# Kernel optimization log

Hardware: AMD Instinct MI355X
Metric: run time of the kernel (lower is better)

The kernel has to match this reference:

```python
import jax, jax.numpy as jnp
import numpy as np

CHUNK = 128  # single steady-state chunk tier (T divisible by 128)
DECAY_MIN = 0.005


def setup_inputs() -> dict:
    key = jax.random.key(0)
    k0, k1, k2, k3, k4 = jax.random.split(key, 5)
    B, H, T, K = 4, 16, 2048, 64
    r = jax.random.normal(k0, (B, H, T, K), jnp.float32) * 0.5
    k = jax.random.normal(k1, (B, H, T, K), jnp.float32) * 0.5
    v = jax.random.normal(k2, (B, H, T, K), jnp.float32)
    # log-space decay (negative); mild magnitude keeps exp() of cumulative
    # in-chunk decays within fp32 range (torch original upcasts to fp64)
    w = -(jax.random.uniform(k3, (B, H, T, K), jnp.float32) * 0.2 + 0.01)
    u = jax.random.normal(k4, (1, H, 1, K), jnp.float32) * 0.5
    wkv_state = jnp.zeros((B, H, K, K), jnp.float32)
    return {"r": r, "k": k, "v": v, "w": w, "u": u, "wkv_state": wkv_state}


def _chunked_wkv(r, k, v, w, u, wkv_state):
    B, H, T, K = r.shape
    Tc = CHUNK
    N = T // Tc
    # decay preprocessing (log space)
    w_decay = jnp.clip(jnp.exp(w), DECAY_MIN, None)
    w_log = jnp.log(w_decay)
    wc = w_log.reshape(B, H, N, Tc, K)
    wc_cum = jnp.cumsum(wc, axis=-2)                       # inclusive cumsum
    shifted = jnp.pad(wc_cum[..., :-1, :], ((0, 0), (0, 0), (0, 0), (1, 0), (0, 0)))
    ws = wc.sum(axis=-2, keepdims=True)                    # (B,H,N,1,K)
    w_inter = jnp.exp(ws - wc_cum)                          # (B,H,N,Tc,K)
    w_intra = jnp.exp(wc_cum - wc)
    ws_e = jnp.exp(jnp.swapaxes(ws, -1, -2))               # (B,H,N,K,1)

    rc = r.reshape(B, H, N, Tc, K)
    kc = k.reshape(B, H, N, Tc, K)
    vc = v.reshape(B, H, N, Tc, K)

    # numerically-centered intra-chunk decays (offset at chunk midpoint)
    off = shifted[..., Tc // 2:Tc // 2 + 1, :]
    r_dec = jnp.exp(shifted - off)
    k_inv = jnp.exp(off - wc_cum)

    # intra-chunk attention: strictly-lower-triangular + u-bonus diagonal
    a = jnp.einsum('bhnik,bhnjk->bhnij', rc * r_dec, kc * k_inv)
    a = jnp.tril(a, -1)
    diag = jnp.einsum('bhntk,bhntk->bhnt', rc, u[:, :, None] * kc)
    a = a + diag[..., :, None] * jnp.eye(Tc, dtype=a.dtype)
    out = jnp.einsum('bhnij,bhnjv->bhniv', a, vc)

    # inter-chunk: sequential state carry via scan
    wkv = jnp.einsum('bhntk,bhntv->bhnkv', kc * w_inter, vc)   # (B,H,N,K,K)

    def step(state, inp):
        ws_i, wkv_i = inp
        return state * ws_i + wkv_i, state

    ws_s = jnp.moveaxis(ws_e, 2, 0)    # (N,B,H,K,1)
    wkv_s = jnp.moveaxis(wkv, 2, 0)    # (N,B,H,K,K)
    final_state, states = jax.lax.scan(step, wkv_state, (ws_s, wkv_s))
    states = jnp.moveaxis(states, 0, 2)  # (B,H,N,K,K) — state entering chunk n

    out = out + jnp.einsum('bhntk,bhnkv->bhntv', rc * w_intra, states)
    return out.reshape(B, H, T, K), final_state


def reference(r, k, v, w, u, wkv_state):
    return _chunked_wkv(r, k, v, w, u, wkv_state)
```

## Files before the change

kernel.cpp:

```cpp
#include <hip/hip_runtime.h>

#define TC 128
#define KD 64
#define WLOG_MIN (-5.2983174f)

typedef __attribute__((ext_vector_type(8))) short short8;
typedef __attribute__((ext_vector_type(4))) short short4_t;
typedef __attribute__((ext_vector_type(4))) float f32x4;

__device__ __forceinline__ unsigned short f2bf(float x) {
  union { float f; unsigned int u; } c; c.f = x;
  unsigned int u = c.u + 0x7fffu + ((c.u >> 16) & 1u);
  return (unsigned short)(u >> 16);
}
__device__ __forceinline__ float bf2f(unsigned short x) {
  union { unsigned int u; float f; } c; c.u = ((unsigned int)x) << 16; return c.f;
}
__device__ __forceinline__ f32x4 shfl4(f32x4 v, int src) {
  f32x4 r;
  #pragma unroll
  for (int i = 0; i < 4; ++i) r[i] = __shfl(v[i], src, 64);
  return r;
}


__global__ __launch_bounds__(512, 8)
void rwkv_wkv(const float* __restrict__ kk_, const float* __restrict__ vv,
              const float* __restrict__ ww,
              unsigned short* __restrict__ wkv_u16, float* __restrict__ wse_ws,
              int N) {
  __shared__ alignas(16) unsigned short vT_s[KD * TC];
  __shared__ alignas(16) unsigned short kiT_s[KD * TC];
  __shared__ alignas(16) float segtot[8 * 64];

  const int bid = blockIdx.x;
  const int n = bid % N, bh = bid / N;
  const size_t base = ((size_t)bh * N + n) * (TC * KD);
  const float *kg = kk_ + base, *vg = vv + base, *wg = ww + base;

  const int tid = threadIdx.x;
  const int lane = tid & 63, wv = tid >> 6;
  const int q = lane >> 4, c4 = lane & 15, kd0 = c4 * 4;

  f32x4 wl4[4];
  #pragma unroll
  for (int j = 0; j < 4; ++j) {
    const int t = wv * 16 + q * 4 + j;
    wl4[j] = *(const f32x4*)&wg[t * KD + kd0];
  }
  #pragma unroll
  for (int j = 0; j < 4; ++j)
    #pragma unroll
    for (int i = 0; i < 4; ++i) wl4[j][i] = fmaxf(wl4[j][i], WLOG_MIN);

  const f32x4 ls = ((wl4[0] + wl4[1]) + wl4[2]) + wl4[3];
  const f32x4 s0 = shfl4(ls, c4), s1 = shfl4(ls, 16 + c4);
  const f32x4 s2 = shfl4(ls, 32 + c4), s3 = shfl4(ls, 48 + c4);
  const f32x4 zero = {0.f, 0.f, 0.f, 0.f};
  f32x4 pre = (q > 0 ? s0 : zero);
  pre += (q > 1 ? s1 : zero);
  pre += (q > 2 ? s2 : zero);
  const f32x4 tot = ((s0 + s1) + s2) + s3;
  if (q == 0) *(f32x4*)&segtot[wv * 64 + kd0] = tot;
  __syncthreads();

  f32x4 segofs4 = zero, myoff4 = zero, wsum4 = zero;
  #pragma unroll
  for (int i = 0; i < 8; ++i) {
    const f32x4 si = *(const f32x4*)&segtot[i * 64 + kd0];
    if (i < wv) segofs4 += si;
    if (i < 4) myoff4 += si;
    wsum4 += si;
  }
  f32x4 wsoff4;
  #pragma unroll
  for (int i = 0; i < 4; ++i) wsoff4[i] = __expf(wsum4[i] - myoff4[i]);
  if (wv == 0 && q == 0) {
    f32x4 e;
    #pragma unroll
    for (int i = 0; i < 4; ++i) e[i] = __expf(wsum4[i]);
    *(f32x4*)&wse_ws[((size_t)bh * N + n) * KD + kd0] = e;
  }

  {
    f32x4 cc = segofs4 + pre;
    short4_t kib[4], vb[4];
    #pragma unroll
    for (int j = 0; j < 4; ++j) {
      const int t = wv * 16 + q * 4 + j;
      const f32x4 k4j = *(const f32x4*)&kg[t * KD + kd0];
      const f32x4 v4j = *(const f32x4*)&vg[t * KD + kd0];
      #pragma unroll
      for (int i = 0; i < 4; ++i) {
        kib[i][j] = (short)f2bf(k4j[i] * __expf(myoff4[i] - cc[i] - wl4[j][i]));
        vb[i][j] = (short)f2bf(v4j[i]);
      }
      cc += wl4[j];
    }
    const int g = wv * 2 + (q >> 1), p4 = (q & 1) * 4;
    #pragma unroll
    for (int i = 0; i < 4; ++i) {
      const int kd = kd0 + i;
      *(short4_t*)&kiT_s[kd * TC + ((g ^ (kd & 7)) << 3) + p4] = kib[i];
      *(short4_t*)&vT_s[kd * TC + ((g ^ (kd & 7)) << 3) + p4] = vb[i];
    }
  }
  __syncthreads();

  {
    const int quad = lane >> 4, l16 = lane & 15;
    const int kt = wv >> 1;
    const int nb = (wv & 1) * 2;
    f32x4 acc[2] = {{0,0,0,0},{0,0,0,0}};
    const int row = kt * 16 + l16;
    #pragma unroll
    for (int ks = 0; ks < 4; ++ks) {
      short8 a = *(const short8*)&kiT_s[row * TC + (((ks * 4 + quad) ^ (row & 7)) << 3)];
      #pragma unroll
      for (int nn = 0; nn < 2; ++nn) {
        const int vd = (nb + nn) * 16 + l16;
        short8 b = *(const short8*)&vT_s[vd * TC + (((ks * 4 + quad) ^ (vd & 7)) << 3)];
        acc[nn] = __builtin_amdgcn_mfma_f32_16x16x32_bf16(a, b, acc[nn], 0, 0, 0);
      }
    }
    float wso[4];
    #pragma unroll
    for (int reg = 0; reg < 4; ++reg) wso[reg] = __shfl(wsoff4[reg], kt * 4 + quad, 64);
    unsigned short* wkvg = wkv_u16 + ((size_t)bh * N + n) * (KD * KD);
    #pragma unroll
    for (int nn = 0; nn < 2; ++nn)
      #pragma unroll
      for (int reg = 0; reg < 4; ++reg)
        wkvg[(kt * 16 + quad * 4 + reg) * KD + (nb + nn) * 16 + l16] = f2bf(acc[nn][reg] * wso[reg]);
  }
}

__global__ __launch_bounds__(512, 4)
void rwkv_main(const float* __restrict__ rr, const float* __restrict__ kk_,
               const float* __restrict__ vv, const float* __restrict__ ww,
               const float* __restrict__ uu,
               const unsigned short* __restrict__ wkv_u16,
               const float* __restrict__ wse_ws,
               const float* __restrict__ st_in,
               float* __restrict__ out, float* __restrict__ final_out,
               int H, int N) {
  __shared__ alignas(16) unsigned short rd_s[TC * KD];
  __shared__ alignas(16) unsigned short ki_s[TC * KD];
  __shared__ alignas(16) unsigned short vT_s[KD * TC];
  __shared__ alignas(16) unsigned short diag_s[TC];
  float* segtot = (float*)rd_s;

  const int bid = blockIdx.x;
  const int n = bid % N, bh = bid / N, h = bh % H;
  const size_t base = ((size_t)bh * N + n) * (TC * KD);
  const float *rg = rr + base, *kg = kk_ + base, *vg = vv + base, *wg = ww + base;

  const int tid = threadIdx.x;
  const int lane = tid & 63, wv = tid >> 6;
  const int q = lane >> 4, c4 = lane & 15, kd0 = c4 * 4;
  const int quad = lane >> 4, l16 = lane & 15;
  const f32x4 uk4 = *(const f32x4*)&uu[h * KD + kd0];

  f32x4 wl4[4], r4[4], k4[4], v4[4];
  #pragma unroll
  for (int j = 0; j < 4; ++j) {
    const int t = wv * 16 + q * 4 + j;
    wl4[j] = *(const f32x4*)&wg[t * KD + kd0];
    r4[j] = *(const f32x4*)&rg[t * KD + kd0];
    k4[j] = *(const f32x4*)&kg[t * KD + kd0];
    v4[j] = *(const f32x4*)&vg[t * KD + kd0];
  }
  #pragma unroll
  for (int j = 0; j < 4; ++j)
    #pragma unroll
    for (int i = 0; i < 4; ++i) wl4[j][i] = fmaxf(wl4[j][i], WLOG_MIN);

  const f32x4 ls = ((wl4[0] + wl4[1]) + wl4[2]) + wl4[3];
  const f32x4 s0 = shfl4(ls, c4), s1 = shfl4(ls, 16 + c4);
  const f32x4 s2 = shfl4(ls, 32 + c4), s3 = shfl4(ls, 48 + c4);
  const f32x4 zero = {0.f, 0.f, 0.f, 0.f};
  f32x4 pre = (q > 0 ? s0 : zero);
  pre += (q > 1 ? s1 : zero);
  pre += (q > 2 ? s2 : zero);
  const f32x4 tot = ((s0 + s1) + s2) + s3;
  if (q == 0) *(f32x4*)&segtot[wv * 64 + kd0] = tot;
  __syncthreads();
  f32x4 segofs4 = zero, myoff4 = zero;
  #pragma unroll
  for (int i = 0; i < 8; ++i) {
    const f32x4 si = *(const f32x4*)&segtot[i * 64 + kd0];
    if (i < wv) segofs4 += si;
    if (i < 4) myoff4 += si;
  }
  __syncthreads();
  f32x4 eoff4;
  #pragma unroll
  for (int i = 0; i < 4; ++i) eoff4[i] = __expf(myoff4[i]);

  short4_t rwq[4];
  {
    f32x4 cc = segofs4 + pre;
    short4_t vb[4];
    float dar[4];
    #pragma unroll
    for (int j = 0; j < 4; ++j) {
      const int t = wv * 16 + q * 4 + j;
      const int addr = t * KD + (((c4 >> 1) ^ (t & 7) ^ ((t >> 3) & 7)) << 3) + (c4 & 1) * 4;
      short4_t rdv, kiv;
      #pragma unroll
      for (int i = 0; i < 4; ++i) {
        const float e1 = __expf(cc[i] - myoff4[i]);
        rdv[i] = (short)f2bf(r4[j][i] * e1);
        rwq[j][i] = (short)f2bf(r4[j][i] * e1 * eoff4[i]);
        kiv[i] = (short)f2bf(k4[j][i] * __expf(myoff4[i] - cc[i] - wl4[j][i]));
        vb[i][j] = (short)f2bf(v4[j][i]);
      }
      *(short4_t*)&rd_s[addr] = rdv;
      *(short4_t*)&ki_s[addr] = kiv;
      dar[j] = r4[j][0] * uk4[0] * k4[j][0];
      dar[j] += r4[j][1] * uk4[1] * k4[j][1];
      dar[j] += r4[j][2] * uk4[2] * k4[j][2];
      dar[j] += r4[j][3] * uk4[3] * k4[j][3];
      cc += wl4[j];
    }
    const int g = wv * 2 + (q >> 1), p4 = (q & 1) * 4;
    #pragma unroll
    for (int i = 0; i < 4; ++i) {
      const int kd = kd0 + i;
      *(short4_t*)&vT_s[kd * TC + ((g ^ (kd & 7)) << 3) + p4] = vb[i];
    }
    #pragma unroll
    for (int o = 8; o > 0; o >>= 1)
      #pragma unroll
      for (int j = 0; j < 4; ++j) dar[j] += __shfl_xor(dar[j], o, 64);
    if (c4 == 0) {
      short4_t dp;
      #pragma unroll
      for (int j = 0; j < 4; ++j) dp[j] = (short)f2bf(dar[j]);
      *(short4_t*)&diag_s[wv * 16 + q * 4] = dp;
    }
  }
  __syncthreads();

  const int skd = tid >> 3, sv0 = (tid & 7) * 8;
  const size_t sbase = (size_t)bh * (KD * KD);
  float s[8];
  *(f32x4*)&s[0] = *(const f32x4*)&st_in[sbase + skd * KD + sv0];
  *(f32x4*)&s[4] = *(const f32x4*)&st_in[sbase + skd * KD + sv0 + 4];
  const float* wseb = wse_ws + (size_t)bh * N * KD + skd;
  const unsigned short* wkvb = wkv_u16 + (size_t)bh * N * (KD * KD) + skd * KD + sv0;
  {
    float e_c = 0.f; short8 x_c = {0};
    if (n > 0) {
      e_c = wseb[0];
      x_c = *(const short8*)&wkvb[0];
    }
    for (int j = 0; j < n; ++j) {
      const float e = e_c; const short8 x = x_c;
      if (j + 1 < n) {
        e_c = wseb[(size_t)(j + 1) * KD];
        x_c = *(const short8*)&wkvb[(size_t)(j + 1) * (KD * KD)];
      }
      #pragma unroll
      for (int i = 0; i < 8; ++i) s[i] = s[i] * e + bf2f((unsigned short)x[i]);
    }
  }

  f32x4 oacc[4];
  {
    const int ib = wv, i0 = ib * 16, irow = i0 + l16;
    const int rsw = (irow & 7) ^ ((irow >> 3) & 7);
    short8 b0 = *(const short8*)&rd_s[irow * KD + ((quad ^ rsw) << 3)];
    short8 b1 = *(const short8*)&rd_s[irow * KD + (((4 + quad) ^ rsw) << 3)];
    const float diag_i = bf2f(diag_s[irow]);
    #pragma unroll
    for (int nn = 0; nn < 4; ++nn) oacc[nn] = (f32x4){0, 0, 0, 0};
    const int npairs = (ib + 2) >> 1;
    unsigned short* astw = &rd_s[wv * 16 * KD];
    for (int jp = 0; jp < npairs; ++jp) {
      #pragma unroll
      for (int jj = 0; jj < 2; ++jj) {
        const int j = jp * 2 + jj;
        short4_t pk;
        if (j <= ib) {
          const int jrow = j * 16 + l16;
          const int jsw = (jrow & 7) ^ ((jrow >> 3) & 7);
          short8 a0 = *(const short8*)&ki_s[jrow * KD + ((quad ^ jsw) << 3)];
          short8 a1 = *(const short8*)&ki_s[jrow * KD + (((4 + quad) ^ jsw) << 3)];
          f32x4 at = {0, 0, 0, 0};
          at = __builtin_amdgcn_mfma_f32_16x16x32_bf16(a0, b0, at, 0, 0, 0);
          at = __builtin_amdgcn_mfma_f32_16x16x32_bf16(a1, b1, at, 0, 0, 0);
          #pragma unroll
          for (int reg = 0; reg < 4; ++reg) {
            const int je = j * 16 + quad * 4 + reg;
            float val = at[reg];
            if (j == ib) val = (je < irow) ? val : ((je == irow) ? diag_i : 0.f);
            pk[reg] = (short)f2bf(val);
          }
        } else {
          pk = (short4_t)0;
        }
        *(short4_t*)&astw[l16 * 40 + jj * 16 + quad * 4] = pk;
      }
      short8 af = *(const short8*)&astw[l16 * 40 + quad * 8];
      #pragma unroll
      for (int nn = 0; nn < 4; ++nn) {
        const int vd = nn * 16 + l16;
        short8 bv = *(const short8*)&vT_s[vd * TC + (((jp * 4 + quad) ^ (vd & 7)) << 3)];
        oacc[nn] = __builtin_amdgcn_mfma_f32_16x16x32_bf16(af, bv, oacc[nn], 0, 0, 0);
      }
    }
  }
  __syncthreads();

  {
    const int g = skd >> 3, k7 = skd & 7;
    #pragma unroll
    for (int i = 0; i < 8; ++i) {
      const int vd = sv0 + i;
      ki_s[vd * KD + (((g ^ (vd & 7)) << 3) | k7)] = f2bf(s[i]);
    }
  }
  #pragma unroll
  for (int j = 0; j < 4; ++j) {
    const int t = wv * 16 + q * 4 + j;
    const int addr = t * KD + (((c4 >> 1) ^ (t & 7) ^ ((t >> 3) & 7)) << 3) + (c4 & 1) * 4;
    *(short4_t*)&rd_s[addr] = rwq[j];
  }
  if (n == N - 1) {
    const float e = wseb[(size_t)n * KD];
    const short8 x = *(const short8*)&wkvb[(size_t)n * (KD * KD)];
    #pragma unroll
    for (int i = 0; i < 8; ++i) s[i] = s[i] * e + bf2f((unsigned short)x[i]);
    *(f32x4*)&final_out[sbase + skd * KD + sv0] = *(const f32x4*)&s[0];
    *(f32x4*)&final_out[sbase + skd * KD + sv0 + 4] = *(const f32x4*)&s[4];
  }
  __syncthreads();

  {
    const int ib = wv, trow = ib * 16 + l16;
    const int rsw = (trow & 7) ^ ((trow >> 3) & 7);
    short8 a0 = *(const short8*)&rd_s[trow * KD + ((quad ^ rsw) << 3)];
    short8 a1 = *(const short8*)&rd_s[trow * KD + (((4 + quad) ^ rsw) << 3)];
    float* og = out + base;
    #pragma unroll
    for (int nn = 0; nn < 4; ++nn) {
      const int vd = nn * 16 + l16;
      short8 b0 = *(const short8*)&ki_s[vd * KD + ((quad ^ (vd & 7)) << 3)];
      short8 b1 = *(const short8*)&ki_s[vd * KD + (((4 + quad) ^ (vd & 7)) << 3)];
      f32x4 acc = {0, 0, 0, 0};
      acc = __builtin_amdgcn_mfma_f32_16x16x32_bf16(a0, b0, acc, 0, 0, 0);
      acc = __builtin_amdgcn_mfma_f32_16x16x32_bf16(a1, b1, acc, 0, 0, 0);
      #pragma unroll
      for (int reg = 0; reg < 4; ++reg)
        og[(size_t)(ib * 16 + quad * 4 + reg) * KD + nn * 16 + l16] = oacc[nn][reg] + acc[reg];
    }
  }
}

extern "C" void kernel_launch(void* const* d_in, const int* in_sizes, int n_in,
                              void* d_out, int out_size, void* d_ws, size_t ws_size,
                              hipStream_t stream) {
  const float* r = (const float*)d_in[0];
  const float* k = (const float*)d_in[1];
  const float* v = (const float*)d_in[2];
  const float* w = (const float*)d_in[3];
  const float* u = (const float*)d_in[4];
  const float* st0 = (const float*)d_in[5];
  float* out = (float*)d_out;

  const int BH = in_sizes[5] / (KD * KD);
  const int H = in_sizes[4] / KD;
  const int T = in_sizes[0] / (BH * KD);
  const int N = T / TC;

  unsigned short* wkv_u16 = (unsigned short*)d_ws;
  float* wse_ws = (float*)(wkv_u16 + (size_t)BH * N * KD * KD);
  float* final_out = out + (size_t)in_sizes[0];

  rwkv_wkv<<<BH * N, 512, 0, stream>>>(k, v, w, wkv_u16, wse_ws, N);
  rwkv_main<<<BH * N, 512, 0, stream>>>(r, k, v, w, u, wkv_u16, wse_ws, st0,
                                        out, final_out, H, N);
}
```

Baseline: 204.2 us.

## Process two consecutive chunks per block to halve state prefix recomputation

Each main-kernel block now handles a pair of adjacent chunks, rebuilding the carried state once for the first chunk and advancing it by one step for the second. This cuts the grid in half and roughly halves the redundant sequential state-prefix loads and FMAs summed over all blocks. In exchange the chunks inside a block run serially with extra barriers, and there are half as many blocks to hide latency (1024 to 512 blocks). The code assumes N is even.

```diff
diff --git a/kernel.cpp b/kernel.cpp
--- a/kernel.cpp
+++ b/kernel.cpp
@@ -150,97 +150,16 @@
   __shared__ alignas(16) unsigned short diag_s[TC];
   float* segtot = (float*)rd_s;
 
+  const int np = N >> 1;
   const int bid = blockIdx.x;
-  const int n = bid % N, bh = bid / N, h = bh % H;
-  const size_t base = ((size_t)bh * N + n) * (TC * KD);
-  const float *rg = rr + base, *kg = kk_ + base, *vg = vv + base, *wg = ww + base;
+  const int p = bid % np, bh = bid / np, h = bh % H;
+  const int n0 = 2 * p, n1 = n0 + 1;
 
   const int tid = threadIdx.x;
   const int lane = tid & 63, wv = tid >> 6;
   const int q = lane >> 4, c4 = lane & 15, kd0 = c4 * 4;
   const int quad = lane >> 4, l16 = lane & 15;
   const f32x4 uk4 = *(const f32x4*)&uu[h * KD + kd0];
-
-  f32x4 wl4[4], r4[4], k4[4], v4[4];
-  #pragma unroll
-  for (int j = 0; j < 4; ++j) {
-    const int t = wv * 16 + q * 4 + j;
-    wl4[j] = *(const f32x4*)&wg[t * KD + kd0];
-    r4[j] = *(const f32x4*)&rg[t * KD + kd0];
-    k4[j] = *(const f32x4*)&kg[t * KD + kd0];
-    v4[j] = *(const f32x4*)&vg[t * KD + kd0];
-  }
-  #pragma unroll
-  for (int j = 0; j < 4; ++j)
-    #pragma unroll
-    for (int i = 0; i < 4; ++i) wl4[j][i] = fmaxf(wl4[j][i], WLOG_MIN);
-
-  const f32x4 ls = ((wl4[0] + wl4[1]) + wl4[2]) + wl4[3];
-  const f32x4 s0 = shfl4(ls, c4), s1 = shfl4(ls, 16 + c4);
-  const f32x4 s2 = shfl4(ls, 32 + c4), s3 = shfl4(ls, 48 + c4);
-  const f32x4 zero = {0.f, 0.f, 0.f, 0.f};
-  f32x4 pre = (q > 0 ? s0 : zero);
-  pre += (q > 1 ? s1 : zero);
-  pre += (q > 2 ? s2 : zero);
-  const f32x4 tot = ((s0 + s1) + s2) + s3;
-  if (q == 0) *(f32x4*)&segtot[wv * 64 + kd0] = tot;
-  __syncthreads();
-  f32x4 segofs4 = zero, myoff4 = zero;
-  #pragma unroll
-  for (int i = 0; i < 8; ++i) {
-    const f32x4 si = *(const f32x4*)&segtot[i * 64 + kd0];
-    if (i < wv) segofs4 += si;
-    if (i < 4) myoff4 += si;
-  }
-  __syncthreads();
-  f32x4 eoff4;
-  #pragma unroll
-  for (int i = 0; i < 4; ++i) eoff4[i] = __expf(myoff4[i]);
-
-  short4_t rwq[4];
-  {
-    f32x4 cc = segofs4 + pre;
-    short4_t vb[4];
-    float dar[4];
-    #pragma unroll
-    for (int j = 0; j < 4; ++j) {
-      const int t = wv * 16 + q * 4 + j;
-      const int addr = t * KD + (((c4 >> 1) ^ (t & 7) ^ ((t >> 3) & 7)) << 3) + (c4 & 1) * 4;
-      short4_t rdv, kiv;
-      #pragma unroll
-      for (int i = 0; i < 4; ++i) {
-        const float e1 = __expf(cc[i] - myoff4[i]);
-        rdv[i] = (short)f2bf(r4[j][i] * e1);
-        rwq[j][i] = (short)f2bf(r4[j][i] * e1 * eoff4[i]);
-        kiv[i] = (short)f2bf(k4[j][i] * __expf(myoff4[i] - cc[i] - wl4[j][i]));
-        vb[i][j] = (short)f2bf(v4[j][i]);
-      }
-      *(short4_t*)&rd_s[addr] = rdv;
-      *(short4_t*)&ki_s[addr] = kiv;
-      dar[j] = r4[j][0] * uk4[0] * k4[j][0];
-      dar[j] += r4[j][1] * uk4[1] * k4[j][1];
-      dar[j] += r4[j][2] * uk4[2] * k4[j][2];
-      dar[j] += r4[j][3] * uk4[3] * k4[j][3];
-      cc += wl4[j];
-    }
-    const int g = wv * 2 + (q >> 1), p4 = (q & 1) * 4;
-    #pragma unroll
-    for (int i = 0; i < 4; ++i) {
-      const int kd = kd0 + i;
-      *(short4_t*)&vT_s[kd * TC + ((g ^ (kd & 7)) << 3) + p4] = vb[i];
-    }
-    #pragma unroll
-    for (int o = 8; o > 0; o >>= 1)
-      #pragma unroll
-      for (int j = 0; j < 4; ++j) dar[j] += __shfl_xor(dar[j], o, 64);
-    if (c4 == 0) {
-      short4_t dp;
-      #pragma unroll
-      for (int j = 0; j < 4; ++j) dp[j] = (short)f2bf(dar[j]);
-      *(short4_t*)&diag_s[wv * 16 + q * 4] = dp;
-    }
-  }
-  __syncthreads();
 
   const int skd = tid >> 3, sv0 = (tid & 7) * 8;
   const size_t sbase = (size_t)bh * (KD * KD);
@@ -251,13 +170,13 @@
   const unsigned short* wkvb = wkv_u16 + (size_t)bh * N * (KD * KD) + skd * KD + sv0;
   {
     float e_c = 0.f; short8 x_c = {0};
-    if (n > 0) {
+    if (n0 > 0) {
       e_c = wseb[0];
       x_c = *(const short8*)&wkvb[0];
     }
-    for (int j = 0; j < n; ++j) {
+    for (int j = 0; j < n0; ++j) {
       const float e = e_c; const short8 x = x_c;
-      if (j + 1 < n) {
+      if (j + 1 < n0) {
         e_c = wseb[(size_t)(j + 1) * KD];
         x_c = *(const short8*)&wkvb[(size_t)(j + 1) * (KD * KD)];
       }
@@ -265,96 +184,193 @@
       for (int i = 0; i < 8; ++i) s[i] = s[i] * e + bf2f((unsigned short)x[i]);
     }
   }
-
-  f32x4 oacc[4];
-  {
-    const int ib = wv, i0 = ib * 16, irow = i0 + l16;
-    const int rsw = (irow & 7) ^ ((irow >> 3) & 7);
-    short8 b0 = *(const short8*)&rd_s[irow * KD + ((quad ^ rsw) << 3)];
-    short8 b1 = *(const short8*)&rd_s[irow * KD + (((4 + quad) ^ rsw) << 3)];
-    const float diag_i = bf2f(diag_s[irow]);
-    #pragma unroll
-    for (int nn = 0; nn < 4; ++nn) oacc[nn] = (f32x4){0, 0, 0, 0};
-    const int npairs = (ib + 2) >> 1;
-    unsigned short* astw = &rd_s[wv * 16 * KD];
-    for (int jp = 0; jp < npairs; ++jp) {
-      #pragma unroll
-      for (int jj = 0; jj < 2; ++jj) {
-        const int j = jp * 2 + jj;
-        short4_t pk;
-        if (j <= ib) {
-          const int jrow = j * 16 + l16;
-          const int jsw = (jrow & 7) ^ ((jrow >> 3) & 7);
-          short8 a0 = *(const short8*)&ki_s[jrow * KD + ((quad ^ jsw) << 3)];
-          short8 a1 = *(const short8*)&ki_s[jrow * KD + (((4 + quad) ^ jsw) << 3)];
-          f32x4 at = {0, 0, 0, 0};
-          at = __builtin_amdgcn_mfma_f32_16x16x32_bf16(a0, b0, at, 0, 0, 0);
-          at = __builtin_amdgcn_mfma_f32_16x16x32_bf16(a1, b1, at, 0, 0, 0);
-          #pragma unroll
-          for (int reg = 0; reg < 4; ++reg) {
-            const int je = j * 16 + quad * 4 + reg;
-            float val = at[reg];
-            if (j == ib) val = (je < irow) ? val : ((je == irow) ? diag_i : 0.f);
-            pk[reg] = (short)f2bf(val);
+  const float en0 = wseb[(size_t)n0 * KD];
+  const short8 xn0 = *(const short8*)&wkvb[(size_t)n0 * (KD * KD)];
+
+  auto do_chunk = [&](int n, const float* s8) {
+    const size_t base = ((size_t)bh * N + n) * (TC * KD);
+    const float *rg = rr + base, *kg = kk_ + base, *vg = vv + base, *wg = ww + base;
+
+    f32x4 wl4[4], r4[4], k4[4], v4[4];
+    #pragma unroll
+    for (int j = 0; j < 4; ++j) {
+      const int t = wv * 16 + q * 4 + j;
+      wl4[j] = *(const f32x4*)&wg[t * KD + kd0];
+      r4[j] = *(const f32x4*)&rg[t * KD + kd0];
+      k4[j] = *(const f32x4*)&kg[t * KD + kd0];
+      v4[j] = *(const f32x4*)&vg[t * KD + kd0];
+    }
+    #pragma unroll
+    for (int j = 0; j < 4; ++j)
+      #pragma unroll
+      for (int i = 0; i < 4; ++i) wl4[j][i] = fmaxf(wl4[j][i], WLOG_MIN);
+
+    const f32x4 ls = ((wl4[0] + wl4[1]) + wl4[2]) + wl4[3];
+    const f32x4 s0 = shfl4(ls, c4), s1 = shfl4(ls, 16 + c4);
+    const f32x4 s2 = shfl4(ls, 32 + c4), s3 = shfl4(ls, 48 + c4);
+    const f32x4 zero = {0.f, 0.f, 0.f, 0.f};
+    f32x4 pre = (q > 0 ? s0 : zero);
+    pre += (q > 1 ? s1 : zero);
+    pre += (q > 2 ? s2 : zero);
+    const f32x4 tot = ((s0 + s1) + s2) + s3;
+    if (q == 0) *(f32x4*)&segtot[wv * 64 + kd0] = tot;
+    __syncthreads();
+    f32x4 segofs4 = zero, myoff4 = zero;
+    #pragma unroll
+    for (int i = 0; i < 8; ++i) {
+      const f32x4 si = *(const f32x4*)&segtot[i * 64 + kd0];
+      if (i < wv) segofs4 += si;
+      if (i < 4) myoff4 += si;
+    }
+    __syncthreads();
+    f32x4 eoff4;
+    #pragma unroll
+    for (int i = 0; i < 4; ++i) eoff4[i] = __expf(myoff4[i]);
+
+    short4_t rwq[4];
+    {
+      f32x4 cc = segofs4 + pre;
+      short4_t vb[4];
+      float dar[4];
+      #pragma unroll
+      for (int j = 0; j < 4; ++j) {
+        const int t = wv * 16 + q * 4 + j;
+        const int addr = t * KD + (((c4 >> 1) ^ (t & 7) ^ ((t >> 3) & 7)) << 3) + (c4 & 1) * 4;
+        short4_t rdv, kiv;
+        #pragma unroll
+        for (int i = 0; i < 4; ++i) {
+          const float e1 = __expf(cc[i] - myoff4[i]);
+          rdv[i] = (short)f2bf(r4[j][i] * e1);
+          rwq[j][i] = (short)f2bf(r4[j][i] * e1 * eoff4[i]);
+          kiv[i] = (short)f2bf(k4[j][i] * __expf(myoff4[i] - cc[i] - wl4[j][i]));
+          vb[i][j] = (short)f2bf(v4[j][i]);
+        }
+        *(short4_t*)&rd_s[addr] = rdv;
+        *(short4_t*)&ki_s[addr] = kiv;
+        dar[j] = r4[j][0] * uk4[0] * k4[j][0];
+        dar[j] += r4[j][1] * uk4[1] * k4[j][1];
+        dar[j] += r4[j][2] * uk4[2] * k4[j][2];
+        dar[j] += r4[j][3] * uk4[3] * k4[j][3];
+        cc += wl4[j];
+      }
+      const int g = wv * 2 + (q >> 1), p4 = (q & 1) * 4;
+      #pragma unroll
+      for (int i = 0; i < 4; ++i) {
+        const int kd = kd0 + i;
+        *(short4_t*)&vT_s[kd * TC + ((g ^ (kd & 7)) << 3) + p4] = vb[i];
+      }
+      #pragma unroll
+      for (int o = 8; o > 0; o >>= 1)
+        #pragma unroll
+        for (int j = 0; j < 4; ++j) dar[j] += __shfl_xor(dar[j], o, 64);
+      if (c4 == 0) {
+        short4_t dp;
+        #pragma unroll
+        for (int j = 0; j < 4; ++j) dp[j] = (short)f2bf(dar[j]);
+        *(short4_t*)&diag_s[wv * 16 + q * 4] = dp;
+      }
+    }
+    __syncthreads();
+
+    f32x4 oacc[4];
+    {
+      const int ib = wv, i0 = ib * 16, irow = i0 + l16;
+      const int rsw = (irow & 7) ^ ((irow >> 3) & 7);
+      short8 b0 = *(const short8*)&rd_s[irow * KD + ((quad ^ rsw) << 3)];
+      short8 b1 = *(const short8*)&rd_s[irow * KD + (((4 + quad) ^ rsw) << 3)];
+      const float diag_i = bf2f(diag_s[irow]);
+      #pragma unroll
+      for (int nn = 0; nn < 4; ++nn) oacc[nn] = (f32x4){0, 0, 0, 0};
+      const int npairs = (ib + 2) >> 1;
+      unsigned short* astw = &rd_s[wv * 16 * KD];
+      for (int jp = 0; jp < npairs; ++jp) {
+        #pragma unroll
+        for (int jj = 0; jj < 2; ++jj) {
+          const int j = jp * 2 + jj;
+          short4_t pk;
+          if (j <= ib) {
+            const int jrow = j * 16 + l16;
+            const int jsw = (jrow & 7) ^ ((jrow >> 3) & 7);
+            short8 a0 = *(const short8*)&ki_s[jrow * KD + ((quad ^ jsw) << 3)];
+            short8 a1 = *(const short8*)&ki_s[jrow * KD + (((4 + quad) ^ jsw) << 3)];
+            f32x4 at = {0, 0, 0, 0};
+            at = __builtin_amdgcn_mfma_f32_16x16x32_bf16(a0, b0, at, 0, 0, 0);
+            at = __builtin_amdgcn_mfma_f32_16x16x32_bf16(a1, b1, at, 0, 0, 0);
+            #pragma unroll
+            for (int reg = 0; reg < 4; ++reg) {
+              const int je = j * 16 + quad * 4 + reg;
+              float val = at[reg];
+              if (j == ib) val = (je < irow) ? val : ((je == irow) ? diag_i : 0.f);
+              pk[reg] = (short)f2bf(val);
+            }
+          } else {
+            pk = (short4_t)0;
           }
-        } else {
-          pk = (short4_t)0;
+          *(short4_t*)&astw[l16 * 40 + jj * 16 + quad * 4] = pk;
         }
-        *(short4_t*)&astw[l16 * 40 + jj * 16 + quad * 4] = pk;
-      }
-      short8 af = *(const short8*)&astw[l16 * 40 + quad * 8];
+        short8 af = *(const short8*)&astw[l16 * 40 + quad * 8];
+        #pragma unroll
+        for (int nn = 0; nn < 4; ++nn) {
+          const int vd = nn * 16 + l16;
+          short8 bv = *(const short8*)&vT_s[vd * TC + (((jp * 4 + quad) ^ (vd & 7)) << 3)];
+          oacc[nn] = __builtin_amdgcn_mfma_f32_16x16x32_bf16(af, bv, oacc[nn], 0, 0, 0);
+        }
+      }
+    }
+    __syncthreads();
+
+    {
+      const int g = skd >> 3, k7 = skd & 7;
+      #pragma unroll
+      for (int i = 0; i < 8; ++i) {
+        const int vd = sv0 + i;
+        ki_s[vd * KD + (((g ^ (vd & 7)) << 3) | k7)] = f2bf(s8[i]);
+      }
+    }
+    #pragma unroll
+    for (int j = 0; j < 4; ++j) {
+      const int t = wv * 16 + q * 4 + j;
+      const int addr = t * KD + (((c4 >> 1) ^ (t & 7) ^ ((t >> 3) & 7)) << 3) + (c4 & 1) * 4;
+      *(short4_t*)&rd_s[addr] = rwq[j];
+    }
+    __syncthreads();
+
+    {
+      const int ib = wv, trow = ib * 16 + l16;
+      const int rsw = (trow & 7) ^ ((trow >> 3) & 7);
+      short8 a0 = *(const short8*)&rd_s[trow * KD + ((quad ^ rsw) << 3)];
+      short8 a1 = *(const short8*)&rd_s[trow * KD + (((4 + quad) ^ rsw) << 3)];
+      float* og = out + base;
       #pragma unroll
       for (int nn = 0; nn < 4; ++nn) {
         const int vd = nn * 16 + l16;
-        short8 bv = *(const short8*)&vT_s[vd * TC + (((jp * 4 + quad) ^ (vd & 7)) << 3)];
-        oacc[nn] = __builtin_amdgcn_mfma_f32_16x16x32_bf16(af, bv, oacc[nn], 0, 0, 0);
-      }
-    }
-  }
-  __syncthreads();
-
-  {
-    const int g = skd >> 3, k7 = skd & 7;
-    #pragma unroll
-    for (int i = 0; i < 8; ++i) {
-      const int vd = sv0 + i;
-      ki_s[vd * KD + (((g ^ (vd & 7)) << 3) | k7)] = f2bf(s[i]);
-    }
-  }
-  #pragma unroll
-  for (int j = 0; j < 4; ++j) {
-    const int t = wv * 16 + q * 4 + j;
-    const int addr = t * KD + (((c4 >> 1) ^ (t & 7) ^ ((t >> 3) & 7)) << 3) + (c4 & 1) * 4;
-    *(short4_t*)&rd_s[addr] = rwq[j];
-  }
-  if (n == N - 1) {
-    const float e = wseb[(size_t)n * KD];
-    const short8 x = *(const short8*)&wkvb[(size_t)n * (KD * KD)];
+        short8 b0 = *(const short8*)&ki_s[vd * KD + ((quad ^ (vd & 7)) << 3)];
+        short8 b1 = *(const short8*)&ki_s[vd * KD + (((4 + quad) ^ (vd & 7)) << 3)];
+        f32x4 acc = {0, 0, 0, 0};
+        acc = __builtin_amdgcn_mfma_f32_16x16x32_bf16(a0, b0, acc, 0, 0, 0);
+        acc = __builtin_amdgcn_mfma_f32_16x16x32_bf16(a1, b1, acc, 0, 0, 0);
+        #pragma unroll
+        for (int reg = 0; reg < 4; ++reg)
+          og[(size_t)(ib * 16 + quad * 4 + reg) * KD + nn * 16 + l16] = oacc[nn][reg] + acc[reg];
+      }
+    }
+    __syncthreads();
+  };
+
+  do_chunk(n0, s);
+
+  #pragma unroll
+  for (int i = 0; i < 8; ++i) s[i] = s[i] * en0 + bf2f((unsigned short)xn0[i]);
+
+  do_chunk(n1, s);
+
+  if (n1 == N - 1) {
+    const float e = wseb[(size_t)n1 * KD];
+    const short8 x = *(const short8*)&wkvb[(size_t)n1 * (KD * KD)];
     #pragma unroll
     for (int i = 0; i < 8; ++i) s[i] = s[i] * e + bf2f((unsigned short)x[i]);
     *(f32x4*)&final_out[sbase + skd * KD + sv0] = *(const f32x4*)&s[0];
     *(f32x4*)&final_out[sbase + skd * KD + sv0 + 4] = *(const f32x4*)&s[4];
-  }
-  __syncthreads();
-
-  {
-    const int ib = wv, trow = ib * 16 + l16;
-    const int rsw = (trow & 7) ^ ((trow >> 3) & 7);
-    short8 a0 = *(const short8*)&rd_s[trow * KD + ((quad ^ rsw) << 3)];
-    short8 a1 = *(const short8*)&rd_s[trow * KD + (((4 + quad) ^ rsw) << 3)];
-    float* og = out + base;
-    #pragma unroll
-    for (int nn = 0; nn < 4; ++nn) {
-      const int vd = nn * 16 + l16;
-      short8 b0 = *(const short8*)&ki_s[vd * KD + ((quad ^ (vd & 7)) << 3)];
-      short8 b1 = *(const short8*)&ki_s[vd * KD + (((4 + quad) ^ (vd & 7)) << 3)];
-      f32x4 acc = {0, 0, 0, 0};
-      acc = __builtin_amdgcn_mfma_f32_16x16x32_bf16(a0, b0, acc, 0, 0, 0);
-      acc = __builtin_amdgcn_mfma_f32_16x16x32_bf16(a1, b1, acc, 0, 0, 0);
-      #pragma unroll
-      for (int reg = 0; reg < 4; ++reg)
-        og[(size_t)(ib * 16 + quad * 4 + reg) * KD + nn * 16 + l16] = oacc[nn][reg] + acc[reg];
-    }
   }
 }
 
@@ -379,6 +395,6 @@
   float* final_out = out + (size_t)in_sizes[0];
 
   rwkv_wkv<<<BH * N, 512, 0, stream>>>(k, v, w, wkv_u16, wse_ws, N);
-  rwkv_main<<<BH * N, 512, 0, stream>>>(r, k, v, w, u, wkv_u16, wse_ws, st0,
-                                        out, final_out, H, N);
-}
+  rwkv_main<<<BH * (N / 2), 512, 0, stream>>>(r, k, v, w, u, wkv_u16, wse_ws,
+                                              st0, out, final_out, H, N);
+}
```

Result: slower. 218.4 us (+7.0%).
